# Kernel optimization log

Hardware: AMD Instinct MI355X
Metric: run time of the kernel (lower is better)

Reference implementation:

```python
import jax, jax.numpy as jnp
import numpy as np
from jax.ops import segment_sum

N_NODES = 100000
N_EDGES = 1600000
N_GRAPHS = 128
HIDDEN = 128
N_CLASSES = 10


def setup_inputs() -> dict:
    key = jax.random.key(0)
    ks = jax.random.split(key, 8)
    src = jax.random.randint(ks[0], (N_EDGES,), 0, N_NODES, dtype=jnp.int32)
    dst = jax.random.randint(ks[1], (N_EDGES,), 0, N_NODES, dtype=jnp.int32)
    graph_ids = jnp.sort(jax.random.randint(ks[2], (N_NODES,), 0, N_GRAPHS, dtype=jnp.int32))
    W1 = jax.random.normal(ks[3], (1, HIDDEN), dtype=jnp.float32)
    b1 = jnp.zeros((HIDDEN,), jnp.float32)
    W2 = jax.random.normal(ks[4], (HIDDEN, HIDDEN), dtype=jnp.float32) * 0.05
    b2 = jnp.zeros((HIDDEN,), jnp.float32)
    Wc = jax.random.normal(ks[5], (HIDDEN, N_CLASSES), dtype=jnp.float32) * 0.05
    bc = jnp.zeros((N_CLASSES,), jnp.float32)
    return {"src": src, "dst": dst, "graph_ids": graph_ids,
            "W1": W1, "b1": b1, "W2": W2, "b2": b2, "Wc": Wc, "bc": bc}


def _graph_conv(h, src, dst, norm_src, norm_dst, W, b, n_nodes):
    # DGL GraphConv, norm='both': D_out^{-1/2} gather -> scatter-sum -> W -> D_in^{-1/2} -> +b
    hs = h * norm_src[:, None]
    agg = segment_sum(hs[src], dst, num_segments=n_nodes)  # [N, F_in]
    return agg @ W * norm_dst[:, None] + b


def reference(src, dst, graph_ids, W1, b1, W2, b2, Wc, bc):
    n_nodes = graph_ids.shape[0]
    ones_e = jnp.ones(src.shape[0], jnp.float32)
    indeg = segment_sum(ones_e, dst, num_segments=n_nodes)
    outdeg = segment_sum(ones_e, src, num_segments=n_nodes)
    norm_src = jnp.clip(outdeg, 1.0, None) ** -0.5
    norm_dst = jnp.clip(indeg, 1.0, None) ** -0.5

    h = indeg[:, None]  # node feature = in-degree, [N, 1]
    h = jax.nn.relu(_graph_conv(h, src, dst, norm_src, norm_dst, W1, b1, n_nodes))
    h = jax.nn.relu(_graph_conv(h, src, dst, norm_src, norm_dst, W2, b2, n_nodes))

    # dgl.mean_nodes: per-graph mean pooling
    sums = segment_sum(h, graph_ids, num_segments=N_GRAPHS)          # [G, H]
    cnts = segment_sum(jnp.ones(n_nodes, jnp.float32), graph_ids, num_segments=N_GRAPHS)
    hg = sums / jnp.clip(cnts, 1.0, None)[:, None]
    return hg @ Wc + bc  # [G, n_classes]
```

## Files before the change

kernel.cpp:

```cpp
#include <hip/hip_runtime.h>

#define N_NODES   100000
#define N_EDGES   1600000
#define N_GRAPHS  128
#define HIDDEN    128
#define N_CLASSES 10

#define BSH   9
#define BSZ   512
#define NBUCK 196
#define CAP   16384
#define PCH   4096

typedef unsigned int   uint;
typedef unsigned short ushort;
typedef unsigned char  uchar;

__global__ __launch_bounds__(256)
void k_part(const int* __restrict__ src, const int* __restrict__ dst,
            unsigned* __restrict__ bcur1, unsigned* __restrict__ bcur2,
            unsigned* __restrict__ tmp1, ushort* __restrict__ tmp2, int nE) {
    __shared__ unsigned histD[256], histS[256], scanT[256];
    __shared__ unsigned lcurD[256], lcurS[256], baseD[256], baseS[256];
    __shared__ unsigned stag1[PCH];
    __shared__ ushort   stag2[PCH];
    __shared__ uchar    stagB1[PCH], stagB2[PCH];
    int t = threadIdx.x;
    int e0 = blockIdx.x * PCH;
    int e1 = min(e0 + PCH, nE);
    histD[t] = 0; histS[t] = 0;
    __syncthreads();
    for (int e = e0 + t; e < e1; e += 256) {
        atomicAdd(&histD[dst[e] >> BSH], 1u);
        atomicAdd(&histS[src[e] >> BSH], 1u);
    }
    __syncthreads();
    unsigned vD = histD[t];
    scanT[t] = vD; __syncthreads();
    for (int off = 1; off < 256; off <<= 1) {
        unsigned add = (t >= off) ? scanT[t - off] : 0u;
        __syncthreads();
        scanT[t] += add;
        __syncthreads();
    }
    unsigned exD = scanT[t] - vD;
    if (vD > 0) { unsigned g = atomicAdd(&bcur1[t], vD); baseD[t] = (unsigned)t * CAP + g - exD; }
    lcurD[t] = exD;
    __syncthreads();
    unsigned vS = histS[t];
    scanT[t] = vS; __syncthreads();
    for (int off = 1; off < 256; off <<= 1) {
        unsigned add = (t >= off) ? scanT[t - off] : 0u;
        __syncthreads();
        scanT[t] += add;
        __syncthreads();
    }
    unsigned exS = scanT[t] - vS;
    if (vS > 0) { unsigned g = atomicAdd(&bcur2[t], vS); baseS[t] = (unsigned)t * CAP + g - exS; }
    lcurS[t] = exS;
    __syncthreads();
    for (int e = e0 + t; e < e1; e += 256) {
        int d = dst[e], s = src[e];
        int bd = d >> BSH, bs = s >> BSH;
        unsigned p1 = atomicAdd(&lcurD[bd], 1u);
        stag1[p1]  = ((unsigned)(d & (BSZ - 1)) << 17) | (unsigned)s;
        stagB1[p1] = (uchar)bd;
        unsigned p2 = atomicAdd(&lcurS[bs], 1u);
        stag2[p2]  = (ushort)(s & (BSZ - 1));
        stagB2[p2] = (uchar)bs;
    }
    __syncthreads();
    int cntE = e1 - e0;
    for (int i = t; i < cntE; i += 256) {
        unsigned b = stagB1[i];
        unsigned a = baseD[b] + (unsigned)i;
        if (a < (b + 1u) * CAP) tmp1[a] = stag1[i];
    }
    for (int i = t; i < cntE; i += 256) {
        unsigned b = stagB2[i];
        unsigned a = baseS[b] + (unsigned)i;
        if (a < (b + 1u) * CAP) tmp2[a] = stag2[i];
    }
}

__global__ __launch_bounds__(1024)
void k_ind_csr(const unsigned* __restrict__ bcur1, const unsigned* __restrict__ tmp1,
               const unsigned* __restrict__ bcur2, const ushort* __restrict__ tmp2,
               unsigned* __restrict__ indeg, float* __restrict__ ns,
               float* __restrict__ hs0, int* __restrict__ rs,
               int* __restrict__ csr) {
    __shared__ unsigned cin[BSZ], cout[BSZ], pref[BSZ], lcur[BSZ];
    int b = blockIdx.x, t = threadIdx.x;
    if (t < BSZ) { cin[t] = 0; cout[t] = 0; }
    __syncthreads();
    unsigned f1 = min(bcur1[b], (unsigned)CAP);
    const unsigned* tp1 = tmp1 + (size_t)b * CAP;
    for (unsigned i = t; i < f1; i += 1024) atomicAdd(&cin[tp1[i] >> 17], 1u);
    unsigned f2 = min(bcur2[b], (unsigned)CAP);
    const ushort* tp2 = tmp2 + (size_t)b * CAP;
    for (unsigned i = t; i < f2; i += 1024) atomicAdd(&cout[tp2[i]], 1u);
    __syncthreads();
    unsigned v = (t < BSZ) ? cin[t] : 0u;
    if (t < BSZ) pref[t] = v;
    __syncthreads();
    for (int off = 1; off < BSZ; off <<= 1) {
        unsigned add = (t < BSZ && t >= off) ? pref[t - off] : 0u;
        __syncthreads();
        if (t < BSZ) pref[t] += add;
        __syncthreads();
    }
    if (t < BSZ) {
        unsigned excl = pref[t] - v;
        lcur[t] = excl;
        int n = b * BSZ + t;
        if (n < N_NODES) {
            unsigned ci = cin[t], co = cout[t];
            float nsv = rsqrtf(fmaxf((float)co, 1.0f));
            indeg[n] = ci;
            ns[n]    = nsv;
            hs0[n]   = (float)ci * nsv;
            rs[n]    = (int)(b * CAP + excl);
        }
    }
    __syncthreads();
    int* cb = csr + (size_t)b * CAP;
    for (unsigned i = t; i < f1; i += 1024) {
        unsigned e = tp1[i];
        unsigned pos = atomicAdd(&lcur[e >> 17], 1u);
        cb[pos] = (int)(e & 0x1FFFFu);
    }
}

__global__ void k_segtable(const float* __restrict__ W1, const float* __restrict__ b1,
                           const float* __restrict__ W2,
                           float* __restrict__ U, float* __restrict__ V,
                           float* __restrict__ ts) {
    __shared__ float s[128];
    int t = threadIdx.x;
    {
        float w = W1[t], bb = b1[t];
        s[t] = (w != 0.0f) ? (-bb / w) : 1e30f;
    }
    __syncthreads();
    for (int k = 2; k <= 128; k <<= 1) {
        for (int j = k >> 1; j > 0; j >>= 1) {
            int ixj = t ^ j;
            if (ixj > t) {
                float a = s[t], bb = s[ixj];
                bool up = ((t & k) == 0);
                if (up ? (a > bb) : (a < bb)) { s[t] = bb; s[ixj] = a; }
            }
            __syncthreads();
        }
    }
    if (blockIdx.x == 0) ts[t] = s[t];
    int sg = blockIdx.x;
    float a_rep;
    if (sg == 0)        a_rep = s[0]   - 1.0f;
    else if (sg == 128) a_rep = s[127] + 1.0f;
    else                a_rep = 0.5f * (s[sg - 1] + s[sg]);
    float u = 0.0f, v = 0.0f;
    for (int j = 0; j < 128; ++j) {
        float w = W1[j], bb = b1[j];
        if (a_rep * w + bb > 0.0f) {
            float w2 = W2[j * HIDDEN + t];
            u += w * w2;
            v += bb * w2;
        }
    }
    U[sg * HIDDEN + t] = u;
    V[sg * HIDDEN + t] = v;
}

__global__ __launch_bounds__(256)
void k_conv1_info(const int* __restrict__ rs, const int* __restrict__ csr,
                  const float* __restrict__ hs0, const unsigned* __restrict__ indeg,
                  const float* __restrict__ ns, const float* __restrict__ ts,
                  float4* __restrict__ info, int nN) {
    __shared__ float sts[128];
    if (threadIdx.x < 128) sts[threadIdx.x] = ts[threadIdx.x];
    __syncthreads();
    int n = blockIdx.x * 256 + threadIdx.x;
    if (n >= nN) return;
    int r0 = rs[n];
    int c  = (int)indeg[n];
    float a = 0.0f;
    #pragma unroll 4
    for (int k = 0; k < c; ++k) a += hs0[csr[r0 + k]];
    float nd = rsqrtf(fmaxf((float)c, 1.0f));
    a *= nd;
    float nsv = ns[n];
    int sg = 0;
    #pragma unroll
    for (int j = 0; j < 128; ++j) sg += (sts[j] < a) ? 1 : 0;
    info[n] = make_float4(nsv * a, nsv, __int_as_float(sg), nd);
}

__global__ __launch_bounds__(256)
void k_conv2_pool(const int* __restrict__ rs, const int* __restrict__ csr,
                  const float4* __restrict__ info, const unsigned* __restrict__ indeg,
                  const float* __restrict__ U, const float* __restrict__ V,
                  const int* __restrict__ graph_ids, const float* __restrict__ b2,
                  float* __restrict__ pool, float* __restrict__ cnt, int nN) {
    __shared__ float sA[256], sB[256], sND[256];
    __shared__ int   sSg[256], sGr[256], sR[256], sC[256];
    int blockBase = blockIdx.x * 256;
    int t = threadIdx.x;
    int n = blockBase + t;

    if (n < nN) {
        int r0 = rs[n], c = (int)indeg[n];
        float A = 0.0f, B = 0.0f;
        int mn = 255, mx = 0;
        #pragma unroll 4
        for (int k = 0; k < c; ++k) {
            float4 nf = info[csr[r0 + k]];
            int sg = __float_as_int(nf.z);
            A += nf.x; B += nf.y;
            mn = min(mn, sg); mx = max(mx, sg);
        }
        sA[t] = A; sB[t] = B;
        sSg[t] = (mn << 8) | mx;
        sR[t] = r0; sC[t] = c;
        sND[t] = info[n].w;
        sGr[t] = graph_ids[n];
    }
    __syncthreads();

    int w = t >> 6, lane = t & 63;
    int n0 = blockBase + 64 * w;
    if (n0 >= nN) return;
    int n1 = min(n0 + 64, nN);

    float bb0 = b2[lane], bb1 = b2[64 + lane];
    int gcur = -1;
    float racc0 = 0.0f, racc1 = 0.0f, cl = 0.0f;

    for (int node = n0; node < n1; ++node) {
        int i = node - blockBase;
        int pk = sSg[i], mn = pk >> 8, mx = pk & 255;
        float acc0, acc1;
        if (mn >= mx) {
            int sg = min(mn, 128);
            float A = sA[i], B = sB[i];
            const float* Ur = U + sg * HIDDEN;
            const float* Vr = V + sg * HIDDEN;
            acc0 = A * Ur[lane]      + B * Vr[lane];
            acc1 = A * Ur[64 + lane] + B * Vr[64 + lane];
        } else {
            acc0 = 0.0f; acc1 = 0.0f;
            int r0 = sR[i], c = sC[i];
            for (int k = 0; k < c; ++k) {
                float4 nf = info[csr[r0 + k]];
                int sg = __float_as_int(nf.z);
                const float* Ur = U + sg * HIDDEN;
                const float* Vr = V + sg * HIDDEN;
                acc0 += nf.x * Ur[lane]      + nf.y * Vr[lane];
                acc1 += nf.x * Ur[64 + lane] + nf.y * Vr[64 + lane];
            }
        }
        float nd = sND[i];
        float r0v = fmaxf(nd * acc0 + bb0, 0.0f);
        float r1v = fmaxf(nd * acc1 + bb1, 0.0f);
        int g = sGr[i];
        if (g != gcur) {
            if (gcur >= 0) {
                atomicAdd(&pool[gcur * HIDDEN + lane],      racc0);
                atomicAdd(&pool[gcur * HIDDEN + 64 + lane], racc1);
                if (lane == 0) atomicAdd(&cnt[gcur], cl);
            }
            gcur = g; racc0 = 0.0f; racc1 = 0.0f; cl = 0.0f;
        }
        racc0 += r0v; racc1 += r1v; cl += 1.0f;
    }
    if (gcur >= 0) {
        atomicAdd(&pool[gcur * HIDDEN + lane],      racc0);
        atomicAdd(&pool[gcur * HIDDEN + 64 + lane], racc1);
        if (lane == 0) atomicAdd(&cnt[gcur], cl);
    }
}

__global__ void k_final(const float* __restrict__ pool, const float* __restrict__ cnt,
                        const float* __restrict__ Wc, const float* __restrict__ bc,
                        float* __restrict__ out) {
    int t = blockIdx.x * blockDim.x + threadIdx.x;
    if (t >= N_GRAPHS * N_CLASSES) return;
    int g = t / N_CLASSES, c = t % N_CLASSES;
    float inv = 1.0f / fmaxf(cnt[g], 1.0f);
    float acc = bc[c];
    for (int j = 0; j < HIDDEN; ++j)
        acc += pool[g * HIDDEN + j] * inv * Wc[j * N_CLASSES + c];
    out[t] = acc;
}

extern "C" void kernel_launch(void* const* d_in, const int* in_sizes, int n_in,
                              void* d_out, int out_size, void* d_ws, size_t ws_size,
                              hipStream_t stream) {
    const int*   src       = (const int*)d_in[0];
    const int*   dst       = (const int*)d_in[1];
    const int*   graph_ids = (const int*)d_in[2];
    const float* W1        = (const float*)d_in[3];
    const float* b1        = (const float*)d_in[4];
    const float* W2        = (const float*)d_in[5];
    const float* b2        = (const float*)d_in[6];
    const float* Wc        = (const float*)d_in[7];
    const float* bc        = (const float*)d_in[8];
    float* out = (float*)d_out;

    char* ws = (char*)d_ws;
    size_t off = 0;
    auto alloc = [&](size_t elems) { void* p = ws + off; off += elems * 4; return p; };

    unsigned* bcur1 = (unsigned*)alloc(256);
    unsigned* bcur2 = (unsigned*)alloc(256);
    float*    pool  = (float*)   alloc(N_GRAPHS * HIDDEN);
    float*    cnt   = (float*)   alloc(N_GRAPHS);
    size_t zero_bytes = off;
    float4*   info  = (float4*)  alloc((size_t)N_NODES * 4);
    unsigned* tmp1  = (unsigned*)alloc((size_t)NBUCK * CAP);
    ushort*   tmp2  = (ushort*)  alloc((size_t)NBUCK * CAP / 2);
    int*      csr   = (int*)     alloc((size_t)NBUCK * CAP);
    int*      rs    = (int*)     alloc(N_NODES);
    unsigned* indeg = (unsigned*)alloc(N_NODES);
    float*    nsA   = (float*)   alloc(N_NODES);
    float*    hs0   = (float*)   alloc(N_NODES);
    float*    ts    = (float*)   alloc(128);
    float*    U     = (float*)   alloc(129 * HIDDEN);
    float*    V     = (float*)   alloc(129 * HIDDEN);

    hipMemsetAsync(d_ws, 0, zero_bytes, stream);

    int pblocks = (N_EDGES + PCH - 1) / PCH;
    int nblocks = (N_NODES + 255) / 256;
    k_part      <<<pblocks, 256, 0, stream>>>(src, dst, bcur1, bcur2, tmp1, tmp2, N_EDGES);
    k_ind_csr   <<<NBUCK, 1024, 0, stream>>>(bcur1, tmp1, bcur2, tmp2, indeg, nsA, hs0, rs, csr);
    k_segtable  <<<129, 128, 0, stream>>>(W1, b1, W2, U, V, ts);
    k_conv1_info<<<nblocks, 256, 0, stream>>>(rs, csr, hs0, indeg, nsA, ts, info, N_NODES);
    k_conv2_pool<<<nblocks, 256, 0, stream>>>(rs, csr, info, indeg, U, V, graph_ids, b2, pool, cnt, N_NODES);
    k_final     <<<(N_GRAPHS * N_CLASSES + 255) / 256, 256, 0, stream>>>(pool, cnt, Wc, bc, out);
}
```

Baseline: 191.2 us.

## Fuse segment-table build into conv1 kernel and split partition passes to cut LDS

```diff
diff --git a/kernel.cpp b/kernel.cpp
--- a/kernel.cpp
+++ b/kernel.cpp
@@ -11,75 +11,92 @@
 #define NBUCK 196
 #define CAP   16384
 #define PCH   4096
+#define PTH   512
 
 typedef unsigned int   uint;
 typedef unsigned short ushort;
 typedef unsigned char  uchar;
 
-__global__ __launch_bounds__(256)
+__global__ __launch_bounds__(PTH)
 void k_part(const int* __restrict__ src, const int* __restrict__ dst,
             unsigned* __restrict__ bcur1, unsigned* __restrict__ bcur2,
             unsigned* __restrict__ tmp1, ushort* __restrict__ tmp2, int nE) {
-    __shared__ unsigned histD[256], histS[256], scanT[256];
-    __shared__ unsigned lcurD[256], lcurS[256], baseD[256], baseS[256];
-    __shared__ unsigned stag1[PCH];
-    __shared__ ushort   stag2[PCH];
-    __shared__ uchar    stagB1[PCH], stagB2[PCH];
+    __shared__ unsigned hist[256], scanT[256], lcur[256], base[256];
+    __shared__ unsigned stag4[PCH];
+    __shared__ uchar    stagB[PCH];
     int t = threadIdx.x;
     int e0 = blockIdx.x * PCH;
     int e1 = min(e0 + PCH, nE);
-    histD[t] = 0; histS[t] = 0;
-    __syncthreads();
-    for (int e = e0 + t; e < e1; e += 256) {
-        atomicAdd(&histD[dst[e] >> BSH], 1u);
-        atomicAdd(&histS[src[e] >> BSH], 1u);
-    }
-    __syncthreads();
-    unsigned vD = histD[t];
-    scanT[t] = vD; __syncthreads();
+    int cntE = e1 - e0;
+
+    if (t < 256) hist[t] = 0;
+    __syncthreads();
+    for (int e = e0 + t; e < e1; e += PTH)
+        atomicAdd(&hist[dst[e] >> BSH], 1u);
+    __syncthreads();
+    unsigned v = (t < 256) ? hist[t] : 0u;
+    if (t < 256) scanT[t] = v;
+    __syncthreads();
     for (int off = 1; off < 256; off <<= 1) {
-        unsigned add = (t >= off) ? scanT[t - off] : 0u;
-        __syncthreads();
-        scanT[t] += add;
-        __syncthreads();
-    }
-    unsigned exD = scanT[t] - vD;
-    if (vD > 0) { unsigned g = atomicAdd(&bcur1[t], vD); baseD[t] = (unsigned)t * CAP + g - exD; }
-    lcurD[t] = exD;
-    __syncthreads();
-    unsigned vS = histS[t];
-    scanT[t] = vS; __syncthreads();
+        unsigned add = (t < 256 && t >= off) ? scanT[t - off] : 0u;
+        __syncthreads();
+        if (t < 256) scanT[t] += add;
+        __syncthreads();
+    }
+    if (t < 256) {
+        unsigned excl = scanT[t] - v;
+        lcur[t] = excl;
+        if (v > 0) { unsigned g = atomicAdd(&bcur1[t], v); base[t] = (unsigned)t * CAP + g - excl; }
+    }
+    __syncthreads();
+    for (int e = e0 + t; e < e1; e += PTH) {
+        int d = dst[e], s = src[e];
+        int b = d >> BSH;
+        unsigned p = atomicAdd(&lcur[b], 1u);
+        stag4[p] = ((unsigned)(d & (BSZ - 1)) << 17) | (unsigned)s;
+        stagB[p] = (uchar)b;
+    }
+    __syncthreads();
+    for (int i = t; i < cntE; i += PTH) {
+        unsigned b = stagB[i];
+        unsigned a = base[b] + (unsigned)i;
+        if (a < (b + 1u) * CAP) tmp1[a] = stag4[i];
+    }
+    __syncthreads();
+
+    if (t < 256) hist[t] = 0;
+    __syncthreads();
+    for (int e = e0 + t; e < e1; e += PTH)
+        atomicAdd(&hist[src[e] >> BSH], 1u);
+    __syncthreads();
+    v = (t < 256) ? hist[t] : 0u;
+    if (t < 256) scanT[t] = v;
+    __syncthreads();
     for (int off = 1; off < 256; off <<= 1) {
-        unsigned add = (t >= off) ? scanT[t - off] : 0u;
-        __syncthreads();
-        scanT[t] += add;
-        __syncthreads();
-    }
-    unsigned exS = scanT[t] - vS;
-    if (vS > 0) { unsigned g = atomicAdd(&bcur2[t], vS); baseS[t] = (unsigned)t * CAP + g - exS; }
-    lcurS[t] = exS;
-    __syncthreads();
-    for (int e = e0 + t; e < e1; e += 256) {
-        int d = dst[e], s = src[e];
-        int bd = d >> BSH, bs = s >> BSH;
-        unsigned p1 = atomicAdd(&lcurD[bd], 1u);
-        stag1[p1]  = ((unsigned)(d & (BSZ - 1)) << 17) | (unsigned)s;
-        stagB1[p1] = (uchar)bd;
-        unsigned p2 = atomicAdd(&lcurS[bs], 1u);
-        stag2[p2]  = (ushort)(s & (BSZ - 1));
-        stagB2[p2] = (uchar)bs;
-    }
-    __syncthreads();
-    int cntE = e1 - e0;
-    for (int i = t; i < cntE; i += 256) {
-        unsigned b = stagB1[i];
-        unsigned a = baseD[b] + (unsigned)i;
-        if (a < (b + 1u) * CAP) tmp1[a] = stag1[i];
-    }
-    for (int i = t; i < cntE; i += 256) {
-        unsigned b = stagB2[i];
-        unsigned a = baseS[b] + (unsigned)i;
-        if (a < (b + 1u) * CAP) tmp2[a] = stag2[i];
+        unsigned add = (t < 256 && t >= off) ? scanT[t - off] : 0u;
+        __syncthreads();
+        if (t < 256) scanT[t] += add;
+        __syncthreads();
+    }
+    if (t < 256) {
+        unsigned excl = scanT[t] - v;
+        lcur[t] = excl;
+        if (v > 0) { unsigned g = atomicAdd(&bcur2[t], v); base[t] = (unsigned)t * CAP + g - excl; }
+    }
+    __syncthreads();
+    ushort* st2 = (ushort*)stag4;
+    for (int e = e0 + t; e < e1; e += PTH) {
+        int s = src[e];
+        int b = s >> BSH;
+        unsigned p = atomicAdd(&lcur[b], 1u);
+        st2[p]   = (ushort)(s & (BSZ - 1));
+        stagB[p] = (uchar)b;
+    }
+    __syncthreads();
+    for (int i = t; i < cntE; i += PTH) {
+        unsigned b = stagB[i];
+        unsigned a = base[b] + (unsigned)i;
+        if (a < (b + 1u) * CAP) tmp2[a] = st2[i];
     }
 }
 
@@ -131,56 +148,53 @@
     }
 }
 
-__global__ void k_segtable(const float* __restrict__ W1, const float* __restrict__ b1,
-                           const float* __restrict__ W2,
-                           float* __restrict__ U, float* __restrict__ V,
-                           float* __restrict__ ts) {
-    __shared__ float s[128];
-    int t = threadIdx.x;
-    {
-        float w = W1[t], bb = b1[t];
-        s[t] = (w != 0.0f) ? (-bb / w) : 1e30f;
-    }
-    __syncthreads();
-    for (int k = 2; k <= 128; k <<= 1) {
-        for (int j = k >> 1; j > 0; j >>= 1) {
-            int ixj = t ^ j;
-            if (ixj > t) {
-                float a = s[t], bb = s[ixj];
-                bool up = ((t & k) == 0);
-                if (up ? (a > bb) : (a < bb)) { s[t] = bb; s[ixj] = a; }
-            }
-            __syncthreads();
-        }
-    }
-    if (blockIdx.x == 0) ts[t] = s[t];
-    int sg = blockIdx.x;
-    float a_rep;
-    if (sg == 0)        a_rep = s[0]   - 1.0f;
-    else if (sg == 128) a_rep = s[127] + 1.0f;
-    else                a_rep = 0.5f * (s[sg - 1] + s[sg]);
-    float u = 0.0f, v = 0.0f;
-    for (int j = 0; j < 128; ++j) {
-        float w = W1[j], bb = b1[j];
-        if (a_rep * w + bb > 0.0f) {
-            float w2 = W2[j * HIDDEN + t];
-            u += w * w2;
-            v += bb * w2;
-        }
-    }
-    U[sg * HIDDEN + t] = u;
-    V[sg * HIDDEN + t] = v;
-}
-
 __global__ __launch_bounds__(256)
 void k_conv1_info(const int* __restrict__ rs, const int* __restrict__ csr,
                   const float* __restrict__ hs0, const unsigned* __restrict__ indeg,
-                  const float* __restrict__ ns, const float* __restrict__ ts,
+                  const float* __restrict__ ns,
+                  const float* __restrict__ W1, const float* __restrict__ b1,
+                  const float* __restrict__ W2,
+                  float* __restrict__ U, float* __restrict__ V,
                   float4* __restrict__ info, int nN) {
     __shared__ float sts[128];
-    if (threadIdx.x < 128) sts[threadIdx.x] = ts[threadIdx.x];
-    __syncthreads();
-    int n = blockIdx.x * 256 + threadIdx.x;
+    int t = threadIdx.x;
+    if (t < 128) {
+        float w = W1[t], bb = b1[t];
+        sts[t] = (w != 0.0f) ? (-bb / w) : 1e30f;
+    }
+    __syncthreads();
+    for (int k = 2; k <= 128; k <<= 1) {
+        for (int j = k >> 1; j > 0; j >>= 1) {
+            if (t < 128) {
+                int ixj = t ^ j;
+                if (ixj > t) {
+                    float a = sts[t], bb = sts[ixj];
+                    bool up = ((t & k) == 0);
+                    if (up ? (a > bb) : (a < bb)) { sts[t] = bb; sts[ixj] = a; }
+                }
+            }
+            __syncthreads();
+        }
+    }
+    if (blockIdx.x < 129 && t < 128) {
+        int sg = blockIdx.x;
+        float a_rep;
+        if (sg == 0)        a_rep = sts[0]   - 1.0f;
+        else if (sg == 128) a_rep = sts[127] + 1.0f;
+        else                a_rep = 0.5f * (sts[sg - 1] + sts[sg]);
+        float u = 0.0f, vv = 0.0f;
+        for (int j = 0; j < 128; ++j) {
+            float w = W1[j], bb = b1[j];
+            if (a_rep * w + bb > 0.0f) {
+                float w2 = W2[j * HIDDEN + t];
+                u  += w * w2;
+                vv += bb * w2;
+            }
+        }
+        U[sg * HIDDEN + t] = u;
+        V[sg * HIDDEN + t] = vv;
+    }
+    int n = blockIdx.x * 256 + t;
     if (n >= nN) return;
     int r0 = rs[n];
     int c  = (int)indeg[n];
@@ -324,7 +338,6 @@
     unsigned* indeg = (unsigned*)alloc(N_NODES);
     float*    nsA   = (float*)   alloc(N_NODES);
     float*    hs0   = (float*)   alloc(N_NODES);
-    float*    ts    = (float*)   alloc(128);
     float*    U     = (float*)   alloc(129 * HIDDEN);
     float*    V     = (float*)   alloc(129 * HIDDEN);
 
@@ -332,10 +345,9 @@
 
     int pblocks = (N_EDGES + PCH - 1) / PCH;
     int nblocks = (N_NODES + 255) / 256;
-    k_part      <<<pblocks, 256, 0, stream>>>(src, dst, bcur1, bcur2, tmp1, tmp2, N_EDGES);
+    k_part      <<<pblocks, PTH, 0, stream>>>(src, dst, bcur1, bcur2, tmp1, tmp2, N_EDGES);
     k_ind_csr   <<<NBUCK, 1024, 0, stream>>>(bcur1, tmp1, bcur2, tmp2, indeg, nsA, hs0, rs, csr);
-    k_segtable  <<<129, 128, 0, stream>>>(W1, b1, W2, U, V, ts);
-    k_conv1_info<<<nblocks, 256, 0, stream>>>(rs, csr, hs0, indeg, nsA, ts, info, N_NODES);
+    k_conv1_info<<<nblocks, 256, 0, stream>>>(rs, csr, hs0, indeg, nsA, W1, b1, W2, U, V, info, N_NODES);
     k_conv2_pool<<<nblocks, 256, 0, stream>>>(rs, csr, info, indeg, U, V, graph_ids, b2, pool, cnt, N_NODES);
     k_final     <<<(N_GRAPHS * N_CLASSES + 255) / 256, 256, 0, stream>>>(pool, cnt, Wc, bc, out);
 }
```

New measurement: 182.9 us. -4.4%, faster.
